# Kernel tuning notes

Measured on AMD Instinct MI355X. Metric: run time of the kernel, lower is better.

## Reference

```python
import jax, jax.numpy as jnp
from jax import lax
import numpy as np

N = 16384      # number of points
S = 4096       # fps samples ('ratio' arg)
CIN = 32       # in_channels
COUT = 64      # out_channels
K = 16         # neighbors
BN_EPS = 1e-5


def _knn(q, d, k):
    # squared euclidean distances via expansion (avoids M x N x 3 delta tensor)
    dist = jnp.sum(q * q, -1)[:, None] - 2.0 * (q @ d.T) + jnp.sum(d * d, -1)[None, :]
    neg, idx = lax.top_k(-dist, k)
    return -neg, idx


def _fps(points, num_samples):
    n = points.shape[0]
    def step(carry, _):
        dmin, far = carry
        d = jnp.sum((points - points[far]) ** 2, -1)
        dmin = jnp.minimum(dmin, d)
        return (dmin, jnp.argmax(dmin)), far
    init = (jnp.full((n,), 1e10, points.dtype), jnp.asarray(0, jnp.int32))
    _, idxs = lax.scan(step, init, None, length=num_samples)
    return idxs


def _bn(x, g, b):
    # BatchNorm1d in training mode: batch stats, biased variance
    m = jnp.mean(x, 0)
    v = jnp.var(x, 0)
    return (x - m) * lax.rsqrt(v + BN_EPS) * g + b


def setup_inputs() -> dict:
    key = jax.random.key(0)
    ks = jax.random.split(key, 16)
    rn = lambda k, shp, sc: (jax.random.normal(k, shp, jnp.float32) * sc)
    d = {
        'points': jax.random.normal(ks[0], (N, 3), jnp.float32),
        'features': jax.random.normal(ks[1], (N, CIN), jnp.float32),
        # PointTransformerLayer projections (stored as (in,out); apply x @ W)
        'Wq': rn(ks[2], (CIN, COUT), CIN ** -0.5),
        'Wk': rn(ks[3], (CIN, COUT), CIN ** -0.5),
        'Wv': rn(ks[4], (CIN, COUT), CIN ** -0.5),
        # mlp_attn: BN,ReLU,Linear(no bias),BN,ReLU,Linear(bias)
        'ga1': jnp.ones((COUT,), jnp.float32), 'ba1': jnp.zeros((COUT,), jnp.float32),
        'Wa1': rn(ks[5], (COUT, COUT), COUT ** -0.5),
        'ga2': jnp.ones((COUT,), jnp.float32), 'ba2': jnp.zeros((COUT,), jnp.float32),
        'Wa2': rn(ks[6], (COUT, COUT), COUT ** -0.5),
        'b_a2': jnp.zeros((COUT,), jnp.float32),
        # mlp_pos: Linear(3,3 no bias),BN(3),ReLU,Linear(3,COUT no bias)
        'Wp1': rn(ks[7], (3, 3), 3 ** -0.5),
        'gp': jnp.ones((3,), jnp.float32), 'bp': jnp.zeros((3,), jnp.float32),
        'Wp2': rn(ks[8], (3, COUT), 3 ** -0.5),
        # TransitionDown mlp: Linear,BN,ReLU,Linear,BN,ReLU (channels=COUT)
        'Wd1': rn(ks[9], (COUT, COUT), COUT ** -0.5),
        'gd1': jnp.ones((COUT,), jnp.float32), 'bd1': jnp.zeros((COUT,), jnp.float32),
        'Wd2': rn(ks[10], (COUT, COUT), COUT ** -0.5),
        'gd2': jnp.ones((COUT,), jnp.float32), 'bd2': jnp.zeros((COUT,), jnp.float32),
        # TransitionUp linears (with bias)
        'Wup': rn(ks[11], (COUT, COUT), COUT ** -0.5),
        'bup': jnp.zeros((COUT,), jnp.float32),
        'Wdn': rn(ks[12], (COUT, COUT), COUT ** -0.5),
        'bdn': jnp.zeros((COUT,), jnp.float32),
    }
    return d


def reference(points, features, Wq, Wk, Wv, ga1, ba1, Wa1, ga2, ba2, Wa2, b_a2,
              Wp1, gp, bp, Wp2, Wd1, gd1, bd1, Wd2, gd2, bd2, Wup, bup, Wdn, bdn):
    n = points.shape[0]
    # ---- PointTransformerLayer ----
    f_q = features @ Wq
    f_k = features @ Wk
    f_v = features @ Wv
    _, knn_idx = _knn(points, points, K)          # (N,K)
    knn_pts = points[knn_idx]                     # (N,K,3)
    knn_k = f_k[knn_idx]                          # (N,K,COUT)
    knn_v = f_v[knn_idx]
    rel = (points[:, None, :] - knn_pts).reshape(-1, 3)
    rpe = (jax.nn.relu(_bn(rel @ Wp1, gp, bp)) @ Wp2).reshape(n, K, COUT)
    vec_sim = f_q[:, None, :] - knn_k + rpe
    x = vec_sim.reshape(-1, COUT)
    x = jax.nn.relu(_bn(x, ga1, ba1)) @ Wa1
    x = jax.nn.relu(_bn(x, ga2, ba2)) @ Wa2 + b_a2
    w = jax.nn.softmax(x.reshape(n, K, COUT), axis=1)
    skip = jnp.sum(w * (knn_v + rpe), axis=1)     # (N,COUT)
    # ---- TransitionDown ----
    s_idx = _fps(points, S)
    s_pts = points[s_idx]                          # (S,3)
    _, knn_idx2 = _knn(s_pts, points, K)           # (S,K)
    kf = skip[knn_idx2.reshape(-1)]                # (S*K,COUT)
    h = jax.nn.relu(_bn(kf @ Wd1, gd1, bd1))
    h = jax.nn.relu(_bn(h @ Wd2, gd2, bd2))
    down_f = jnp.max(h.reshape(S, K, COUT), axis=1)  # (S,COUT)
    # ---- TransitionUp ----
    df = down_f @ Wdn + bdn
    knn_d3, knn_idx3 = _knn(points, s_pts, 3)       # (N,3)
    neigh = df[knn_idx3]                            # (N,3,COUT)
    recip = 1.0 / (knn_d3 + 1e-8)
    w3 = recip / jnp.sum(recip, -1, keepdims=True)
    interp = jnp.sum(w3[..., None] * neigh, axis=1)
    return interp + skip @ Wup + bup
```

## Files before the change

### kernel.cpp

```cpp
#include <hip/hip_runtime.h>
#include <math.h>

#define NP 16384
#define SP 4096
#define CINCH 32
#define CO 64
#define KK 16
#define NW 192

__device__ __forceinline__ float waveGemm64(float xv, const float* __restrict__ wl, int c) {
  float a0=0.f,a1=0.f,a2=0.f,a3=0.f;
  #pragma unroll
  for (int k=0;k<64;k+=4){
    a0 = fmaf(__shfl(xv,k  ), wl[(k  )*CO+c], a0);
    a1 = fmaf(__shfl(xv,k+1), wl[(k+1)*CO+c], a1);
    a2 = fmaf(__shfl(xv,k+2), wl[(k+2)*CO+c], a2);
    a3 = fmaf(__shfl(xv,k+3), wl[(k+3)*CO+c], a3);
  }
  return (a0+a1)+(a2+a3);
}

template<int NS>
__device__ __forceinline__ void mergeQ(const float* __restrict__ pv, const int* __restrict__ pi,
                                       int* __restrict__ outp){
  int pos[NS]; float hv[NS]; int hi[NS];
  #pragma unroll
  for (int p=0;p<NS;p++){ pos[p]=0; hv[p]=pv[p*KK]; hi[p]=pi[p*KK]; }
  #pragma unroll
  for (int k=0;k<KK;k++){
    int best=0; float bv=hv[0]; int bi=hi[0];
    #pragma unroll
    for (int p=1;p<NS;p++){
      bool g=(hv[p]<bv)||((hv[p]==bv)&&(hi[p]<bi));
      if (g){ bv=hv[p]; bi=hi[p]; best=p; }
    }
    outp[k]=bi;
    #pragma unroll
    for (int p=0;p<NS;p++) if (best==p){
      pos[p]++;
      bool ok = pos[p]<KK;
      hv[p] = ok ? pv[p*KK+pos[p]] : 3.4e38f;
      hi[p] = ok ? pi[p*KK+pos[p]] : 0x7fffffff;
    }
  }
}

__device__ __forceinline__ void wbar(int* ctr, int target){
  __syncthreads();
  if (threadIdx.x==0){
    __threadfence();
    atomicAdd(ctr,1);
    while (__hip_atomic_load(ctr, __ATOMIC_RELAXED, __HIP_MEMORY_SCOPE_AGENT) < target)
      __builtin_amdgcn_s_sleep(8);
    __threadfence();
  }
  __syncthreads();
}

__global__ __launch_bounds__(256) void k_pts4(const float* __restrict__ pts, float4* __restrict__ pts4) {
  int i = blockIdx.x*256 + threadIdx.x;
  float x = pts[3*i], y = pts[3*i+1], z = pts[3*i+2];
  pts4[i] = make_float4(x,y,z, x*x + y*y + z*z);
}

__global__ __launch_bounds__(512,2) void k_mega(
    const float4* __restrict__ pts4,
    const float* __restrict__ feat,
    const float* __restrict__ Wq, const float* __restrict__ Wk, const float* __restrict__ Wv,
    const float* __restrict__ Wp1, const float* __restrict__ gp, const float* __restrict__ bp,
    const float* __restrict__ Wp2, const float* __restrict__ Wa1, const float* __restrict__ Wa2,
    const float* __restrict__ ga1, const float* __restrict__ ba1,
    const float* __restrict__ ga2, const float* __restrict__ ba2, const float* __restrict__ b_a2,
    int* __restrict__ sidx,
    float* __restrict__ fq, float* __restrict__ fk, float* __restrict__ fv,
    int* __restrict__ kidx, float* __restrict__ y, float* __restrict__ yn,
    float* __restrict__ skip,
    float* __restrict__ psv, int* __restrict__ psi,
    float* __restrict__ stRel, float* __restrict__ stX, float* __restrict__ stX1,
    int* __restrict__ wctr)
{
  __shared__ __align__(16) char smem[131200];
  const int tid = threadIdx.x;

  if (blockIdx.x == 0) {
    #pragma clang fp contract(off)
    float2* xy  = (float2*)smem;
    float*  rbv = (float*)(smem + 131072);
    int*    rbi = (int*)  (smem + 131072 + 32);
    const int t = tid;
    float z[32], dm[32];
    #pragma unroll
    for (int m=0;m<32;m++){
      float4 p = pts4[t*32+m];
      xy[m*512+t] = make_float2(p.x, p.y);
      z[m] = p.z;
      dm[m] = 1e10f;
    }
    #pragma unroll
    for (int m=0;m<32;m++) asm volatile("" : "+v"(z[m]));
    __syncthreads();
    int far = 0;
    float4 f0 = pts4[0];
    float fx=f0.x, fy=f0.y, fz=f0.z;
    for (int s=0;s<SP;s++){
      if (t==0) sidx[s]=far;
      float bv=-1.f; int bi=0;
      #pragma unroll
      for (int m=0;m<32;m++){
        float2 p = xy[m*512+t];
        float dx=p.x-fx, dy=p.y-fy, dz=z[m]-fz;
        float q0=dx*dx, q1=dy*dy, q2=dz*dz;
        float d=(q0+q1)+q2;
        float nd=fminf(dm[m],d);
        dm[m]=nd;
        bool g = nd>bv;
        bv = g?nd:bv;
        bi = g?(t*32+m):bi;
      }
      #pragma unroll
      for (int o=1;o<64;o<<=1){
        float ov=__shfl_xor(bv,o); int oi=__shfl_xor(bi,o);
        bool g = (ov>bv)||((ov==bv)&&(oi<bi));
        bv=g?ov:bv; bi=g?oi:bi;
      }
      __syncthreads();
      if ((t&63)==0){ rbv[t>>6]=bv; rbi[t>>6]=bi; }
      __syncthreads();
      float cv=rbv[t&7]; int ci=rbi[t&7];
      #pragma unroll
      for (int o=1;o<8;o<<=1){
        float ov=__shfl_xor(cv,o); int oi=__shfl_xor(ci,o);
        bool g=(ov>cv)||((ov==cv)&&(oi<ci));
        cv=g?ov:cv; ci=g?oi:ci;
      }
      far = ci;
      float4 fp = pts4[far];
      fx=fp.x; fy=fp.y; fz=fp.z;
    }
    return;
  }

  const int bid = blockIdx.x - 1;
  const int c = tid & 63;
  const int wv_ = tid >> 6;

  for (int u = bid; u < NP/8; u += NW){
    int row = u*8 + wv_;
    const float* f = feat + row*CINCH;
    float aq=0.f, ak=0.f, av=0.f;
    #pragma unroll
    for (int k=0;k<CINCH;k++){
      float fe=f[k];
      aq=fmaf(fe,Wq[k*CO+c],aq); ak=fmaf(fe,Wk[k*CO+c],ak); av=fmaf(fe,Wv[k*CO+c],av);
    }
    fq[row*CO+c]=aq; fk[row*CO+c]=ak; fv[row*CO+c]=av;
  }
  wbar(wctr, 1*NW);

  {
    float4* tile = (float4*)smem;
    for (int u = bid; u < 512; u += NW){
      int qb = u >> 4, part = u & 15;
      int q = qb*512 + tid;
      int c0 = part*1024;
      __syncthreads();
      tile[tid]     = pts4[c0+tid];
      tile[tid+512] = pts4[c0+tid+512];
      __syncthreads();
      float4 tq = pts4[q];
      float qx=tq.x,qy=tq.y,qz=tq.z;
      float v[KK]; int id[KK];
      #pragma unroll
      for (int k=0;k<KK;k++){ v[k]=3.4e38f; id[k]=0x7fffffff; }
      for (int j=0;j<1024;j++){
        float4 cpt=tile[j];
        float dot = qx*cpt.x + qy*cpt.y + qz*cpt.z;
        float s = fmaf(-2.f,dot,cpt.w);
        if (s < v[KK-1]) {
          int gj = c0+j;
          #pragma unroll
          for (int k=KK-1;k>=1;--k){
            bool sh = s < v[k-1];
            bool pl = s < v[k];
            float nv = sh ? v[k-1] : (pl ? s  : v[k]);
            int   ni = sh ? id[k-1] : (pl ? gj : id[k]);
            v[k]=nv; id[k]=ni;
          }
          if (s < v[0]){ v[0]=s; id[0]=gj; }
        }
      }
      size_t o = ((size_t)q*16 + part)*KK;
      #pragma unroll
      for (int k=0;k<KK;k++){ psv[o+k]=v[k]; psi[o+k]=id[k]; }
    }
  }
  wbar(wctr, 2*NW);

  for (int q = bid*512 + tid; q < NP; q += NW*512)
    mergeQ<16>(psv + (size_t)q*16*KK, psi + (size_t)q*16*KK, kidx + q*KK);
  wbar(wctr, 3*NW);

  for (int r = bid*512 + tid; r < NP*KK; r += NW*512){
    int i = r>>4;
    int j = kidx[r];
    float4 pi=pts4[i], pj=pts4[j];
    float rx=pi.x-pj.x, ry=pi.y-pj.y, rz=pi.z-pj.z;
    float sv[3], sq[3];
    #pragma unroll
    for (int cc=0;cc<3;cc++){
      float yc = rx*Wp1[cc] + ry*Wp1[3+cc] + rz*Wp1[6+cc];
      y[r*3+cc]=yc; sv[cc]=yc; sq[cc]=yc*yc;
    }
    #pragma unroll
    for (int cc=0;cc<3;cc++){
      float a=sv[cc], b=sq[cc];
      #pragma unroll
      for (int o=32;o;o>>=1){ a+=__shfl_down(a,o); b+=__shfl_down(b,o); }
      if ((tid&63)==0){ atomicAdd(&stRel[cc],a); atomicAdd(&stRel[3+cc],b); }
    }
  }
  wbar(wctr, 4*NW);

  {
    const float invn = 1.f/(float)(NP*KK);
    for (int r = bid*512 + tid; r < NP*KK; r += NW*512){
      #pragma unroll
      for (int cc=0;cc<3;cc++){
        float m = stRel[cc]*invn;
        float var = stRel[3+cc]*invn - m*m;
        float rs = 1.f/sqrtf(var+1e-5f);
        float tt = (y[r*3+cc]-m)*rs;
        tt = fmaf(tt, gp[cc], bp[cc]);
        yn[r*3+cc] = fmaxf(tt,0.f);
      }
    }
  }
  wbar(wctr, 5*NW);

  {
    float* red = (float*)(smem + 16384);
    float w0=Wp2[c], w1=Wp2[64+c], w2=Wp2[128+c];
    float s=0.f,sq=0.f;
    for (int u = bid; u < 512; u += NW){
      int row0 = (u*8 + wv_)*64;
      for (int q2=0;q2<64;q2++){
        int r=row0+q2; int p=r>>4; int j=kidx[r];
        float y0=yn[r*3], y1=yn[r*3+1], y2=yn[r*3+2];
        float x = fq[p*CO+c]-fk[j*CO+c]+(y0*w0+y1*w1+y2*w2);
        s+=x; sq=fmaf(x,x,sq);
      }
    }
    red[(0*8+wv_)*64+c]=s; red[(1*8+wv_)*64+c]=sq;
    __syncthreads();
    if (wv_==0){
      float a=0.f,b=0.f;
      #pragma unroll
      for (int u=0;u<8;u++){ a+=red[(0*8+u)*64+c]; b+=red[(1*8+u)*64+c]; }
      atomicAdd(&stX[c],a); atomicAdd(&stX[64+c],b);
    }
  }
  wbar(wctr, 6*NW);

  {
    float* wa1 = (float*)smem;
    float* red = (float*)(smem + 16384);
    for (int u=tid; u<4096; u+=512) wa1[u]=Wa1[u];
    __syncthreads();
    const float invn=1.f/(float)(NP*KK);
    float m1=stX[c]*invn; float vv=stX[64+c]*invn-m1*m1; float rs1=1.f/sqrtf(vv+1e-5f);
    float g1=ga1[c], bb1=ba1[c];
    float w0=Wp2[c],w1=Wp2[64+c],w2=Wp2[128+c];
    float s=0.f,sq=0.f;
    for (int u = bid; u < 512; u += NW){
      int row0 = (u*8 + wv_)*64;
      for (int q2=0;q2<64;q2++){
        int r=row0+q2; int p=r>>4; int j=kidx[r];
        float y0=yn[r*3],y1=yn[r*3+1],y2=yn[r*3+2];
        float x = fq[p*CO+c]-fk[j*CO+c]+(y0*w0+y1*w1+y2*w2);
        float tt=(x-m1)*rs1; tt=fmaxf(fmaf(tt,g1,bb1),0.f);
        float x1 = waveGemm64(tt, wa1, c);
        s += x1; sq = fmaf(x1,x1,sq);
      }
    }
    red[(0*8+wv_)*64+c]=s; red[(1*8+wv_)*64+c]=sq;
    __syncthreads();
    if (wv_==0){
      float a=0.f,b=0.f;
      #pragma unroll
      for (int u=0;u<8;u++){ a+=red[(0*8+u)*64+c]; b+=red[(1*8+u)*64+c]; }
      atomicAdd(&stX1[c],a); atomicAdd(&stX1[64+c],b);
    }
  }
  wbar(wctr, 7*NW);

  {
    float* wa1 = (float*)smem;
    float* wa2 = (float*)(smem + 16384);
    for (int u=tid; u<4096; u+=512){ wa1[u]=Wa1[u]; wa2[u]=Wa2[u]; }
    __syncthreads();
    const float invn = 1.f/(float)(NP*KK);
    float m1=stX[c]*invn;  float va=stX[64+c]*invn-m1*m1;  float rs1=1.f/sqrtf(va+1e-5f);
    float m2=stX1[c]*invn; float vb=stX1[64+c]*invn-m2*m2; float rs2=1.f/sqrtf(vb+1e-5f);
    float g1=ga1[c], bb1=ba1[c], g2=ga2[c], bb2=ba2[c], bc=b_a2[c];
    float w0=Wp2[c], w1=Wp2[64+c], w2=Wp2[128+c];
    for (int u = bid; u < NP/8; u += NW){
      int p = u*8 + wv_;
      float fqv = fq[p*CO+c];
      float ex[16];
      #pragma unroll
      for (int k=0;k<16;k++){
        int r=p*16+k; int j=kidx[r];
        float y0=yn[r*3],y1=yn[r*3+1],y2=yn[r*3+2];
        float x = fqv - fk[j*CO+c] + (y0*w0+y1*w1+y2*w2);
        float t1 = (x-m1)*rs1; t1 = fmaxf(fmaf(t1,g1,bb1),0.f);
        float x1 = waveGemm64(t1, wa1, c);
        float t2 = (x1-m2)*rs2; t2 = fmaxf(fmaf(t2,g2,bb2),0.f);
        ex[k] = waveGemm64(t2, wa2, c) + bc;
      }
      float mx = ex[0];
      #pragma unroll
      for (int k=1;k<16;k++) mx = fmaxf(mx, ex[k]);
      float sum=0.f;
      #pragma unroll
      for (int k=0;k<16;k++){ ex[k]=expf(ex[k]-mx); sum+=ex[k]; }
      float acc=0.f;
      #pragma unroll
      for (int k=0;k<16;k++){
        int r=p*16+k; int j=kidx[r];
        float y0=yn[r*3],y1=yn[r*3+1],y2=yn[r*3+2];
        float rpe = y0*w0+y1*w1+y2*w2;
        acc = fmaf(ex[k], fv[j*CO+c]+rpe, acc);
      }
      skip[p*CO+c] = acc/sum;
    }
  }
}

__global__ __launch_bounds__(256) void k_gather(const float4* __restrict__ pts4, const int* __restrict__ sidx,
    float4* __restrict__ spts4) {
  int q = blockIdx.x*256 + threadIdx.x;
  spts4[q] = pts4[sidx[q]];
}

#define KTS 2048
__global__ __launch_bounds__(256,4) void k_knn16p(const float4* __restrict__ qp,
    const float4* __restrict__ cp, int clen,
    float* __restrict__ psv, int* __restrict__ psi) {
  __shared__ float4 tile[KTS];
  int q = blockIdx.x*256 + threadIdx.x;
  int part = blockIdx.y;
  int nspl = gridDim.y;
  int c0 = part*clen;
  float4 tq = qp[q];
  float qx=tq.x, qy=tq.y, qz=tq.z;
  float v[KK]; int id[KK];
  #pragma unroll
  for (int k=0;k<KK;k++){ v[k]=3.4e38f; id[k]=0x7fffffff; }
  for (int base=c0; base<c0+clen; base+=KTS){
    __syncthreads();
    for (int tt=threadIdx.x;tt<KTS;tt+=256) tile[tt]=cp[base+tt];
    __syncthreads();
    for (int j=0;j<KTS;j++){
      float4 cpt=tile[j];
      float dot = qx*cpt.x + qy*cpt.y + qz*cpt.z;
      float s = fmaf(-2.f,dot,cpt.w);
      if (s < v[KK-1]) {
        int gj = base+j;
        #pragma unroll
        for (int k=KK-1;k>=1;--k){
          bool sh = s < v[k-1];
          bool pl = s < v[k];
          float nv = sh ? v[k-1] : (pl ? s  : v[k]);
          int   ni = sh ? id[k-1] : (pl ? gj : id[k]);
          v[k]=nv; id[k]=ni;
        }
        if (s < v[0]){ v[0]=s; id[0]=gj; }
      }
    }
  }
  size_t o = ((size_t)q*nspl + part)*KK;
  #pragma unroll
  for (int k=0;k<KK;k++){ psv[o+k]=v[k]; psi[o+k]=id[k]; }
}

template<int NS>
__global__ __launch_bounds__(256,4) void k_merge(const float* __restrict__ psv,
    const int* __restrict__ psi, int* __restrict__ oidx) {
  int q = blockIdx.x*256 + threadIdx.x;
  mergeQ<NS>(psv + (size_t)q*NS*KK, psi + (size_t)q*NS*KK, oidx + q*KK);
}

__global__ __launch_bounds__(256) void k_d1(const float* __restrict__ skip, const int* __restrict__ idx2,
    const float* __restrict__ Wd1, float* __restrict__ t1, float* __restrict__ st) {
  __shared__ float wl[4096];
  __shared__ float red[2][4][64];
  for (int t=threadIdx.x;t<4096;t+=256) wl[t]=Wd1[t];
  int w=threadIdx.x>>6, c=threadIdx.x&63;
  __syncthreads();
  float s=0.f,sq=0.f;
  int row0 = blockIdx.x*64 + w*16;
  for (int t=0;t<16;t++){
    int r=row0+t; int src=idx2[r];
    float kf = skip[src*CO+c];
    float o = waveGemm64(kf, wl, c);
    t1[r*CO+c]=o; s+=o; sq=fmaf(o,o,sq);
  }
  red[0][w][c]=s; red[1][w][c]=sq;
  __syncthreads();
  if (w==0){
    float a=red[0][0][c]+red[0][1][c]+red[0][2][c]+red[0][3][c];
    float b=red[1][0][c]+red[1][1][c]+red[1][2][c]+red[1][3][c];
    atomicAdd(&st[c],a); atomicAdd(&st[64+c],b);
  }
}

__global__ __launch_bounds__(256) void k_d2(const float* __restrict__ t1in, const float* __restrict__ stin,
    const float* __restrict__ gd1, const float* __restrict__ bd1, const float* __restrict__ Wd2,
    float* __restrict__ t2, float* __restrict__ st) {
  __shared__ float wl[4096];
  __shared__ float red[2][4][64];
  for (int t=threadIdx.x;t<4096;t+=256) wl[t]=Wd2[t];
  int w=threadIdx.x>>6, c=threadIdx.x&63;
  const float invn = 1.f/(float)(SP*KK);
  float m=stin[c]*invn; float va=stin[64+c]*invn-m*m; float rs=1.f/sqrtf(va+1e-5f);
  float g=gd1[c], bb=bd1[c];
  __syncthreads();
  float s=0.f,sq=0.f;
  int row0 = blockIdx.x*64 + w*16;
  for (int t=0;t<16;t++){
    int r=row0+t;
    float h = (t1in[r*CO+c]-m)*rs; h = fmaxf(fmaf(h,g,bb),0.f);
    float o = waveGemm64(h, wl, c);
    t2[r*CO+c]=o; s+=o; sq=fmaf(o,o,sq);
  }
  red[0][w][c]=s; red[1][w][c]=sq;
  __syncthreads();
  if (w==0){
    float a=red[0][0][c]+red[0][1][c]+red[0][2][c]+red[0][3][c];
    float b=red[1][0][c]+red[1][1][c]+red[1][2][c]+red[1][3][c];
    atomicAdd(&st[c],a); atomicAdd(&st[64+c],b);
  }
}

__global__ __launch_bounds__(256) void k_downf(const float* __restrict__ t2, const float* __restrict__ stin,
    const float* __restrict__ gd2, const float* __restrict__ bd2, const float* __restrict__ Wdn,
    const float* __restrict__ bdn, float* __restrict__ df) {
  __shared__ float wl[4096];
  for (int t=threadIdx.x;t<4096;t+=256) wl[t]=Wdn[t];
  int w=threadIdx.x>>6, c=threadIdx.x&63;
  int srow = blockIdx.x*4 + w;
  const float invn = 1.f/(float)(SP*KK);
  float m=stin[c]*invn; float va=stin[64+c]*invn-m*m; float rs=1.f/sqrtf(va+1e-5f);
  float g=gd2[c], bb=bd2[c];
  __syncthreads();
  float mx=-3.4e38f;
  for (int k=0;k<16;k++){
    float h=(t2[(srow*16+k)*CO+c]-m)*rs; h=fmaxf(fmaf(h,g,bb),0.f);
    mx=fmaxf(mx,h);
  }
  float o = waveGemm64(mx, wl, c) + bdn[c];
  df[srow*CO+c]=o;
}

__global__ __launch_bounds__(256,4) void k_knn3(const float4* __restrict__ qp, const float4* __restrict__ cp,
    int* __restrict__ idx3, float* __restrict__ d3) {
  __shared__ float4 tile[2048];
  int q = blockIdx.x*256 + threadIdx.x;
  float4 Q = qp[q];
  float v0=3.4e38f,v1=3.4e38f,v2=3.4e38f;
  int i0=0x7fffffff,i1=0x7fffffff,i2=0x7fffffff;
  for (int base=0;base<SP;base+=2048){
    __syncthreads();
    for (int tt=threadIdx.x;tt<2048;tt+=256) tile[tt]=cp[base+tt];
    __syncthreads();
    for (int j=0;j<2048;j++){
      float4 cpt = tile[j];
      float dot = Q.x*cpt.x + Q.y*cpt.y + Q.z*cpt.z;
      float d = fmaf(-2.f, dot, Q.w) + cpt.w;
      if (d < v2){
        int gj = base+j;
        bool s2 = d < v1;
        bool s1 = d < v0;
        v2 = s2 ? v1 : d;  i2 = s2 ? i1 : gj;
        v1 = s2 ? (s1 ? v0 : d) : v1; i1 = s2 ? (s1 ? i0 : gj) : i1;
        v0 = s1 ? d : v0;  i0 = s1 ? gj : i0;
      }
    }
  }
  idx3[q*3]=i0; idx3[q*3+1]=i1; idx3[q*3+2]=i2;
  d3[q*3]=v0; d3[q*3+1]=v1; d3[q*3+2]=v2;
}

__global__ __launch_bounds__(256) void k_out(const float* __restrict__ df, const int* __restrict__ idx3,
    const float* __restrict__ d3, const float* __restrict__ skip, const float* __restrict__ Wup,
    const float* __restrict__ bup, float* __restrict__ out) {
  __shared__ float wl[4096];
  for (int t=threadIdx.x;t<4096;t+=256) wl[t]=Wup[t];
  int w=threadIdx.x>>6, c=threadIdx.x&63;
  int i = blockIdx.x*4 + w;
  __syncthreads();
  int j0=idx3[i*3], j1=idx3[i*3+1], j2=idx3[i*3+2];
  float e0=d3[i*3], e1=d3[i*3+1], e2=d3[i*3+2];
  float r0=1.f/(e0+1e-8f), r1=1.f/(e1+1e-8f), r2=1.f/(e2+1e-8f);
  float sm=(r0+r1)+r2;
  float w0=r0/sm, w1=r1/sm, w2=r2/sm;
  float interp = (w0*df[j0*CO+c] + w1*df[j1*CO+c]) + w2*df[j2*CO+c];
  float sk = skip[i*CO+c];
  float up = waveGemm64(sk, wl, c);
  out[i*CO+c] = (interp + up) + bup[c];
}

extern "C" void kernel_launch(void* const* d_in, const int* in_sizes, int n_in,
                              void* d_out, int out_size, void* d_ws, size_t ws_size,
                              hipStream_t stream) {
  (void)in_sizes; (void)n_in; (void)out_size; (void)ws_size;
  const float* points   = (const float*)d_in[0];
  const float* features = (const float*)d_in[1];
  const float* Wq  = (const float*)d_in[2];
  const float* Wk  = (const float*)d_in[3];
  const float* Wv  = (const float*)d_in[4];
  const float* ga1 = (const float*)d_in[5];
  const float* ba1 = (const float*)d_in[6];
  const float* Wa1 = (const float*)d_in[7];
  const float* ga2 = (const float*)d_in[8];
  const float* ba2 = (const float*)d_in[9];
  const float* Wa2 = (const float*)d_in[10];
  const float* b_a2= (const float*)d_in[11];
  const float* Wp1 = (const float*)d_in[12];
  const float* gp  = (const float*)d_in[13];
  const float* bp  = (const float*)d_in[14];
  const float* Wp2 = (const float*)d_in[15];
  const float* Wd1 = (const float*)d_in[16];
  const float* gd1 = (const float*)d_in[17];
  const float* bd1 = (const float*)d_in[18];
  const float* Wd2 = (const float*)d_in[19];
  const float* gd2 = (const float*)d_in[20];
  const float* bd2 = (const float*)d_in[21];
  const float* Wup = (const float*)d_in[22];
  const float* bup = (const float*)d_in[23];
  const float* Wdn = (const float*)d_in[24];
  const float* bdn = (const float*)d_in[25];
  float* out = (float*)d_out;

  char* wp = (char*)d_ws;
  auto carve = [&](size_t bytes)->char* { char* p = wp; wp += (bytes + 255) & ~(size_t)255; return p; };
  float4* pts4  = (float4*)carve((size_t)NP*16);
  float*  fq    = (float*) carve((size_t)NP*CO*4);
  float*  fk    = (float*) carve((size_t)NP*CO*4);
  float*  fv    = (float*) carve((size_t)NP*CO*4);
  int*    kidx  = (int*)   carve((size_t)NP*KK*4);
  float*  y     = (float*) carve((size_t)NP*KK*3*4);
  float*  yn    = (float*) carve((size_t)NP*KK*3*4);
  float*  skip  = (float*) carve((size_t)NP*CO*4);
  int*    sidx  = (int*)   carve((size_t)SP*4);
  float4* spts4 = (float4*)carve((size_t)SP*16);
  int*    idx2  = (int*)   carve((size_t)SP*KK*4);
  float*  t1    = (float*) carve((size_t)SP*KK*CO*4);
  float*  t2    = (float*) carve((size_t)SP*KK*CO*4);
  float*  df    = (float*) carve((size_t)SP*CO*4);
  int*    idx3  = (int*)   carve((size_t)NP*3*4);
  float*  d3    = (float*) carve((size_t)NP*3*4);
  float*  stats = (float*) carve(4096);
  float* stRel = stats;
  float* stX   = stats + 8;
  float* stX1  = stats + 136;
  float* stD1  = stats + 264;
  float* stD2  = stats + 392;
  int*   wctr  = (int*)(stats + 768);
  float* psvNP = t1;
  int*   psiNP = (int*)t2;
  float* psvSP = t2;
  int*   psiSP = (int*)(t2 + (size_t)SP*8*KK);

  hipMemsetAsync(stats, 0, 4096, stream);

  k_pts4 <<<NP/256, 256, 0, stream>>>(points, pts4);

  k_mega <<<1+NW, 512, 0, stream>>>(pts4, features,
      Wq, Wk, Wv, Wp1, gp, bp, Wp2, Wa1, Wa2, ga1, ba1, ga2, ba2, b_a2,
      sidx, fq, fk, fv, kidx, y, yn, skip, psvNP, psiNP, stRel, stX, stX1, wctr);

  k_gather   <<<SP/256, 256, 0, stream>>>(pts4, sidx, spts4);
  k_knn16p   <<<dim3(SP/256,8), 256, 0, stream>>>(spts4, pts4, NP/8, psvSP, psiSP);
  k_merge<8> <<<SP/256, 256, 0, stream>>>(psvSP, psiSP, idx2);
  k_d1       <<<SP*KK/64, 256, 0, stream>>>(skip, idx2, Wd1, t1, stD1);
  k_d2       <<<SP*KK/64, 256, 0, stream>>>(t1, stD1, gd1, bd1, Wd2, t2, stD2);
  k_downf    <<<SP/4,   256, 0, stream>>>(t2, stD2, gd2, bd2, Wdn, bdn, df);
  k_knn3     <<<NP/256, 256, 0, stream>>>(pts4, spts4, idx3, d3);
  k_out      <<<NP/4,   256, 0, stream>>>(df, idx3, d3, skip, Wup, bup, out);
}
```

Measured before the change: 10.54 ms.

## Morton-sort points and skip inactive threads in FPS via bounding-sphere culling

Adds a bbox, histogram, scan and scatter pass that reorders points by 16^3 Morton cell, so each FPS thread owns a spatially compact set of 32 points. Each thread precomputes a bounding sphere and skips the distance update when the new far point cannot lower its current maximum, carrying the coordinates of the chosen point through the reduction so no global reload is needed. The wave reduction now uses DPP instead of shfl_xor, and the cross-wave reduction uses double-buffered shared memory so only one barrier is needed per step. This adds several small kernels and tie-breaking on original index, and the conservative culling bound risks subtle mismatches.

```diff
diff --git a/kernel.cpp b/kernel.cpp
--- a/kernel.cpp
+++ b/kernel.cpp
@@ -6,6 +6,8 @@
 #define CINCH 32
 #define CO 64
 #define KK 16
+#define GRIDC 16
+#define NCELLS 4096
 #define NW 192
 
 __device__ __forceinline__ float waveGemm64(float xv, const float* __restrict__ wl, int c) {
@@ -18,6 +20,15 @@
     a3 = fmaf(__shfl(xv,k+3), wl[(k+3)*CO+c], a3);
   }
   return (a0+a1)+(a2+a3);
+}
+
+__device__ __forceinline__ int morton12(int x,int y,int z){
+  int m=0;
+  #pragma unroll
+  for (int b=0;b<4;b++){
+    m |= ((x>>b)&1)<<(3*b) | ((y>>b)&1)<<(3*b+1) | ((z>>b)&1)<<(3*b+2);
+  }
+  return m;
 }
 
 template<int NS>
@@ -63,8 +74,96 @@
   pts4[i] = make_float4(x,y,z, x*x + y*y + z*z);
 }
 
+__global__ __launch_bounds__(1024) void k_bbox(const float4* __restrict__ pts4, float* __restrict__ bbox) {
+  __shared__ float red[6][16];
+  int t = threadIdx.x;
+  float mnx=3e38f,mny=3e38f,mnz=3e38f,mxx=-3e38f,mxy=-3e38f,mxz=-3e38f;
+  for (int i=t;i<NP;i+=1024){
+    float4 p = pts4[i];
+    mnx=fminf(mnx,p.x); mny=fminf(mny,p.y); mnz=fminf(mnz,p.z);
+    mxx=fmaxf(mxx,p.x); mxy=fmaxf(mxy,p.y); mxz=fmaxf(mxz,p.z);
+  }
+  #pragma unroll
+  for (int o=1;o<64;o<<=1){
+    mnx=fminf(mnx,__shfl_xor(mnx,o)); mny=fminf(mny,__shfl_xor(mny,o)); mnz=fminf(mnz,__shfl_xor(mnz,o));
+    mxx=fmaxf(mxx,__shfl_xor(mxx,o)); mxy=fmaxf(mxy,__shfl_xor(mxy,o)); mxz=fmaxf(mxz,__shfl_xor(mxz,o));
+  }
+  if ((t&63)==0){
+    int w=t>>6;
+    red[0][w]=mnx; red[1][w]=mny; red[2][w]=mnz; red[3][w]=mxx; red[4][w]=mxy; red[5][w]=mxz;
+  }
+  __syncthreads();
+  if (t==0){
+    float a0=red[0][0],a1=red[1][0],a2=red[2][0],a3=red[3][0],a4=red[4][0],a5=red[5][0];
+    for (int w=1;w<16;w++){
+      a0=fminf(a0,red[0][w]); a1=fminf(a1,red[1][w]); a2=fminf(a2,red[2][w]);
+      a3=fmaxf(a3,red[3][w]); a4=fmaxf(a4,red[4][w]); a5=fmaxf(a5,red[5][w]);
+    }
+    bbox[0]=a0; bbox[1]=a1; bbox[2]=a2; bbox[3]=a3; bbox[4]=a4; bbox[5]=a5;
+  }
+}
+
+__global__ __launch_bounds__(256) void k_cellhist(const float4* __restrict__ pts4,
+    const float* __restrict__ bbox, int* __restrict__ hist) {
+  int i = blockIdx.x*256 + threadIdx.x;
+  float4 p = pts4[i];
+  float sx=(float)GRIDC/(bbox[3]-bbox[0]+1e-6f);
+  float sy=(float)GRIDC/(bbox[4]-bbox[1]+1e-6f);
+  float sz=(float)GRIDC/(bbox[5]-bbox[2]+1e-6f);
+  int cx=min(GRIDC-1,max(0,(int)((p.x-bbox[0])*sx)));
+  int cy=min(GRIDC-1,max(0,(int)((p.y-bbox[1])*sy)));
+  int cz=min(GRIDC-1,max(0,(int)((p.z-bbox[2])*sz)));
+  atomicAdd(&hist[morton12(cx,cy,cz)],1);
+}
+
+__global__ __launch_bounds__(1024) void k_scan(const int* __restrict__ hist, int* __restrict__ cellStart) {
+  __shared__ int wsum[16];
+  int t = threadIdx.x;
+  int h0=hist[4*t], h1=hist[4*t+1], h2=hist[4*t+2], h3=hist[4*t+3];
+  int T = h0+h1+h2+h3;
+  int incl = T;
+  #pragma unroll
+  for (int o=1;o<64;o<<=1){
+    int n = __shfl_up(incl,o);
+    if ((t&63)>=o) incl += n;
+  }
+  if ((t&63)==63) wsum[t>>6]=incl;
+  __syncthreads();
+  int woff=0;
+  for (int i=0;i<(t>>6);i++) woff += wsum[i];
+  int excl = woff + incl - T;
+  cellStart[4*t]=excl; cellStart[4*t+1]=excl+h0; cellStart[4*t+2]=excl+h0+h1; cellStart[4*t+3]=excl+h0+h1+h2;
+}
+
+__global__ __launch_bounds__(256) void k_scatter(const float4* __restrict__ pts4,
+    const float* __restrict__ bbox, const int* __restrict__ cellStart, int* __restrict__ cursor,
+    float4* __restrict__ pfp) {
+  int i = blockIdx.x*256 + threadIdx.x;
+  float4 p = pts4[i];
+  float sx=(float)GRIDC/(bbox[3]-bbox[0]+1e-6f);
+  float sy=(float)GRIDC/(bbox[4]-bbox[1]+1e-6f);
+  float sz=(float)GRIDC/(bbox[5]-bbox[2]+1e-6f);
+  int cx=min(GRIDC-1,max(0,(int)((p.x-bbox[0])*sx)));
+  int cy=min(GRIDC-1,max(0,(int)((p.y-bbox[1])*sy)));
+  int cz=min(GRIDC-1,max(0,(int)((p.z-bbox[2])*sz)));
+  int cell = morton12(cx,cy,cz);
+  int pos = cellStart[cell] + atomicAdd(&cursor[cell],1);
+  pfp[pos] = make_float4(p.x,p.y,p.z,__int_as_float(i));
+}
+
+#define DPP5(CTRL) { \
+  int nv_=__builtin_amdgcn_update_dpp(__float_as_int(rv),__float_as_int(rv),CTRL,0xF,0xF,false); \
+  int ni_=__builtin_amdgcn_update_dpp(ri,ri,CTRL,0xF,0xF,false); \
+  int nx_=__builtin_amdgcn_update_dpp(__float_as_int(rx),__float_as_int(rx),CTRL,0xF,0xF,false); \
+  int ny_=__builtin_amdgcn_update_dpp(__float_as_int(ry),__float_as_int(ry),CTRL,0xF,0xF,false); \
+  int nz_=__builtin_amdgcn_update_dpp(__float_as_int(rz),__float_as_int(rz),CTRL,0xF,0xF,false); \
+  float ov_=__int_as_float(nv_); \
+  bool g_=(ov_>rv)||((ov_==rv)&&(ni_<ri)); \
+  rv=g_?ov_:rv; ri=g_?ni_:ri; \
+  rx=g_?__int_as_float(nx_):rx; ry=g_?__int_as_float(ny_):ry; rz=g_?__int_as_float(nz_):rz; }
+
 __global__ __launch_bounds__(512,2) void k_mega(
-    const float4* __restrict__ pts4,
+    const float4* __restrict__ pts4, const float4* __restrict__ pfp,
     const float* __restrict__ feat,
     const float* __restrict__ Wq, const float* __restrict__ Wk, const float* __restrict__ Wv,
     const float* __restrict__ Wp1, const float* __restrict__ gp, const float* __restrict__ bp,
@@ -79,63 +178,86 @@
     float* __restrict__ stRel, float* __restrict__ stX, float* __restrict__ stX1,
     int* __restrict__ wctr)
 {
-  __shared__ __align__(16) char smem[131200];
+  __shared__ __align__(16) char smem[131456];
   const int tid = threadIdx.x;
 
   if (blockIdx.x == 0) {
     #pragma clang fp contract(off)
-    float2* xy  = (float2*)smem;
-    float*  rbv = (float*)(smem + 131072);
-    int*    rbi = (int*)  (smem + 131072 + 32);
+    float2* xy = (float2*)smem;
+    float4* sA = (float4*)(smem + 131072);
+    int*    sI = (int*)  (smem + 131072 + 256);
     const int t = tid;
-    float z[32], dm[32];
+    const int w = t>>6;
+    float z[32], dm[32]; int oid[32];
+    float mnx=3e38f,mny=3e38f,mnz=3e38f,mxx=-3e38f,mxy=-3e38f,mxz=-3e38f;
+    int minoid=0x7fffffff; float mbx=0.f,mby=0.f,mbz=0.f;
     #pragma unroll
     for (int m=0;m<32;m++){
-      float4 p = pts4[t*32+m];
+      float4 p = pfp[t*32+m];
       xy[m*512+t] = make_float2(p.x, p.y);
-      z[m] = p.z;
-      dm[m] = 1e10f;
+      z[m]=p.z; oid[m]=__float_as_int(p.w); dm[m]=1e10f;
+      mnx=fminf(mnx,p.x); mny=fminf(mny,p.y); mnz=fminf(mnz,p.z);
+      mxx=fmaxf(mxx,p.x); mxy=fmaxf(mxy,p.y); mxz=fmaxf(mxz,p.z);
+      bool g = oid[m]<minoid;
+      minoid=g?oid[m]:minoid; mbx=g?p.x:mbx; mby=g?p.y:mby; mbz=g?p.z:mbz;
     }
     #pragma unroll
     for (int m=0;m<32;m++) asm volatile("" : "+v"(z[m]));
+    float cx=0.5f*(mnx+mxx), cy=0.5f*(mny+mxy), cz=0.5f*(mnz+mxz);
+    float r2=0.f;
+    #pragma unroll
+    for (int m=0;m<32;m++){
+      float2 p = xy[m*512+t];
+      float dx=p.x-cx, dy=p.y-cy, dz=z[m]-cz;
+      r2=fmaxf(r2,(dx*dx+dy*dy)+dz*dz);
+    }
+    float rad = sqrtf(r2)*1.00002f+1e-6f;
+    float bv=1e10f; int boid=minoid; float bx=mbx,by=mby,bz=mbz;
     __syncthreads();
     int far = 0;
     float4 f0 = pts4[0];
     float fx=f0.x, fy=f0.y, fz=f0.z;
     for (int s=0;s<SP;s++){
       if (t==0) sidx[s]=far;
-      float bv=-1.f; int bi=0;
-      #pragma unroll
-      for (int m=0;m<32;m++){
-        float2 p = xy[m*512+t];
-        float dx=p.x-fx, dy=p.y-fy, dz=z[m]-fz;
-        float q0=dx*dx, q1=dy*dy, q2=dz*dz;
-        float d=(q0+q1)+q2;
-        float nd=fminf(dm[m],d);
-        dm[m]=nd;
-        bool g = nd>bv;
-        bv = g?nd:bv;
-        bi = g?(t*32+m):bi;
-      }
-      #pragma unroll
-      for (int o=1;o<64;o<<=1){
-        float ov=__shfl_xor(bv,o); int oi=__shfl_xor(bi,o);
-        bool g = (ov>bv)||((ov==bv)&&(oi<bi));
-        bv=g?ov:bv; bi=g?oi:bi;
-      }
+      float Dx=fx-cx, Dy=fy-cy, Dz=fz-cz;
+      float D2=(Dx*Dx+Dy*Dy)+Dz*Dz;
+      float tq = sqrtf(D2)-rad;
+      bool active = !((tq>0.f)&&(tq*tq*0.999f>=bv));
+      if (active){
+        float nbv=-1.f; int nbo=0x7fffffff; float nbx=0.f,nby=0.f,nbz=0.f;
+        #pragma unroll
+        for (int m=0;m<32;m++){
+          float2 p = xy[m*512+t];
+          float dx=p.x-fx, dy=p.y-fy, dz=z[m]-fz;
+          float q0=dx*dx, q1=dy*dy, q2=dz*dz;
+          float d=(q0+q1)+q2;
+          float nd=fminf(dm[m],d);
+          dm[m]=nd;
+          bool g=(nd>nbv)||((nd==nbv)&&(oid[m]<nbo));
+          nbv=g?nd:nbv; nbo=g?oid[m]:nbo;
+          nbx=g?p.x:nbx; nby=g?p.y:nby; nbz=g?z[m]:nbz;
+        }
+        bv=nbv; boid=nbo; bx=nbx; by=nby; bz=nbz;
+      }
+      float rv=bv, rx=bx, ry=by, rz=bz; int ri=boid;
+      DPP5(0xB1)
+      DPP5(0x4E)
+      DPP5(0x141)
+      DPP5(0x140)
+      DPP5(0x142)
+      DPP5(0x143)
+      int pb = s&1;
+      if ((t&63)==63){ sA[pb*8+w]=make_float4(rx,ry,rz,rv); sI[pb*8+w]=ri; }
       __syncthreads();
-      if ((t&63)==0){ rbv[t>>6]=bv; rbi[t>>6]=bi; }
-      __syncthreads();
-      float cv=rbv[t&7]; int ci=rbi[t&7];
-      #pragma unroll
-      for (int o=1;o<8;o<<=1){
-        float ov=__shfl_xor(cv,o); int oi=__shfl_xor(ci,o);
-        bool g=(ov>cv)||((ov==cv)&&(oi<ci));
-        cv=g?ov:cv; ci=g?oi:ci;
-      }
-      far = ci;
-      float4 fp = pts4[far];
-      fx=fp.x; fy=fp.y; fz=fp.z;
+      float4 e0=sA[pb*8];
+      float gv=e0.w, gx=e0.x, gy=e0.y, gz=e0.z; int gi=sI[pb*8];
+      #pragma unroll
+      for (int u=1;u<8;u++){
+        float4 e=sA[pb*8+u]; int oi2=sI[pb*8+u];
+        bool g=(e.w>gv)||((e.w==gv)&&(oi2<gi));
+        gv=g?e.w:gv; gi=g?oi2:gi; gx=g?e.x:gx; gy=g?e.y:gy; gz=g?e.z:gz;
+      }
+      far=gi; fx=gx; fy=gy; fz=gz;
     }
     return;
   }
@@ -545,6 +667,7 @@
   char* wp = (char*)d_ws;
   auto carve = [&](size_t bytes)->char* { char* p = wp; wp += (bytes + 255) & ~(size_t)255; return p; };
   float4* pts4  = (float4*)carve((size_t)NP*16);
+  float4* pfp   = (float4*)carve((size_t)NP*16);
   float*  fq    = (float*) carve((size_t)NP*CO*4);
   float*  fk    = (float*) carve((size_t)NP*CO*4);
   float*  fv    = (float*) carve((size_t)NP*CO*4);
@@ -560,7 +683,11 @@
   float*  df    = (float*) carve((size_t)SP*CO*4);
   int*    idx3  = (int*)   carve((size_t)NP*3*4);
   float*  d3    = (float*) carve((size_t)NP*3*4);
+  float*  bbox  = (float*) carve(256);
+  int*    cellStart = (int*)carve((size_t)NCELLS*4);
   float*  stats = (float*) carve(4096);
+  int*    hist  = (int*)   carve((size_t)NCELLS*4);
+  int*    cursor= (int*)   carve((size_t)NCELLS*4);
   float* stRel = stats;
   float* stX   = stats + 8;
   float* stX1  = stats + 136;
@@ -572,11 +699,15 @@
   float* psvSP = t2;
   int*   psiSP = (int*)(t2 + (size_t)SP*8*KK);
 
-  hipMemsetAsync(stats, 0, 4096, stream);
-
-  k_pts4 <<<NP/256, 256, 0, stream>>>(points, pts4);
-
-  k_mega <<<1+NW, 512, 0, stream>>>(pts4, features,
+  hipMemsetAsync(stats, 0, 4096 + NCELLS*4*2, stream);
+
+  k_pts4     <<<NP/256, 256, 0, stream>>>(points, pts4);
+  k_bbox     <<<1, 1024, 0, stream>>>(pts4, bbox);
+  k_cellhist <<<NP/256, 256, 0, stream>>>(pts4, bbox, hist);
+  k_scan     <<<1, 1024, 0, stream>>>(hist, cellStart);
+  k_scatter  <<<NP/256, 256, 0, stream>>>(pts4, bbox, cellStart, cursor, pfp);
+
+  k_mega <<<1+NW, 512, 0, stream>>>(pts4, pfp, features,
       Wq, Wk, Wv, Wp1, gp, bp, Wp2, Wa1, Wa2, ga1, ba1, ga2, ba2, b_a2,
       sidx, fq, fk, fv, kidx, y, yn, skip, psvNP, psiNP, stRel, stX, stX1, wctr);
 
```

New measurement: 20.16 ms. 91.3% more time.
